# Performance work log

Measured on AMD Instinct MI355X. Metric: run time of the kernel, lower is better.

## Reference

```python
import jax, jax.numpy as jnp
import numpy as np

B, N, I_IN, O_OUT, S_EX, S_PHI, S_RHO = 1024, 32, 6, 5, 10, 60, 60
N_ACTIONS, N_ROLES = 5, 7


def _gru(x, h, Wih, Whh, bih, bhh):
    # PyTorch GRUCell math
    gi = x @ Wih.T + bih
    gh = h @ Whh.T + bhh
    ir, iz, inn = jnp.split(gi, 3, axis=-1)
    hr, hz, hn = jnp.split(gh, 3, axis=-1)
    r = jax.nn.sigmoid(ir + hr)
    u = jax.nn.sigmoid(iz + hz)
    n = jnp.tanh(inn + r * hn)
    return (1.0 - u) * n + u * h


def setup_inputs():
    key = jax.random.key(0)
    ks = jax.random.split(key, 32)
    has = (jax.random.uniform(ks[0], (B, N)) < 0.8).astype(jnp.float32)  # per-batch node existence
    z = jax.random.normal(ks[1], (B, N, S_EX), jnp.float32)
    dz = jax.random.normal(ks[2], (B, N, S_EX), jnp.float32)
    # union-graph DAG adjacency: adj[j, i] == edge j -> i, j < i (strictly upper triangular)
    adj = jnp.triu(jax.random.uniform(ks[3], (N, N)) < 0.3, k=1)

    def U(k, shape, fan_in):
        s = 1.0 / np.sqrt(fan_in)
        return jax.random.uniform(k, shape, jnp.float32, -s, s)

    fin = S_PHI + 2 * S_EX
    p = {
        'Wih_f': U(ks[4], (3 * S_PHI, S_RHO), S_PHI),
        'Whh_f': U(ks[5], (3 * S_PHI, S_PHI), S_PHI),
        'bih_f': U(ks[6], (3 * S_PHI,), S_PHI),
        'bhh_f': U(ks[7], (3 * S_PHI,), S_PHI),
        'Wih_b': U(ks[8], (3 * S_PHI, S_RHO), S_PHI),
        'Whh_b': U(ks[9], (3 * S_PHI, S_PHI), S_PHI),
        'bih_b': U(ks[10], (3 * S_PHI,), S_PHI),
        'bhh_b': U(ks[11], (3 * S_PHI,), S_PHI),
        'Wf': U(ks[12], (S_RHO, fin), fin), 'bf': U(ks[13], (S_RHO,), fin),
        'Wb': U(ks[14], (S_RHO, fin), fin), 'bb': U(ks[15], (S_RHO,), fin),
        'Wa': U(ks[16], (N_ACTIONS, 2 * S_PHI), 2 * S_PHI), 'ba': U(ks[17], (N_ACTIONS,), 2 * S_PHI),
        'Wc': U(ks[18], (1, 2 * S_PHI), 2 * S_PHI), 'bc': U(ks[19], (1,), 2 * S_PHI),
        'Wu': U(ks[20], (N_ROLES, 2 * S_RHO), 2 * S_RHO), 'bu': U(ks[21], (N_ROLES,), 2 * S_RHO),
    }
    return {'has': has, 'z': z, 'dz': dz, 'adj': adj, **p}


def reference(has, z, dz, adj,
              Wih_f, Whh_f, bih_f, bhh_f,
              Wih_b, Whh_b, bih_b, bhh_b,
              Wf, bf, Wb, bb, Wa, ba, Wc, bc, Wu, bu):
    adjf = adj.astype(z.dtype)

    # ---- forward message pass over DAG (ascending node order) ----
    def fwd_node(rho_f, i):
        def step(h, j):
            m = adjf[j, i] * has[:, j][:, None]  # interpolate mask: edge exists AND source node exists
            h2 = _gru(rho_f[j], h, Wih_f, Whh_f, bih_f, bhh_f)
            return h + m * (h2 - h), None
        h, _ = jax.lax.scan(step, jnp.zeros((B, S_PHI), z.dtype), jnp.arange(N))
        rho_i = jnp.tanh(jnp.concatenate([h, z[:, i], dz[:, i]], 1) @ Wf.T + bf)
        return rho_f.at[i].set(rho_i), None

    rho_f, _ = jax.lax.scan(fwd_node, jnp.zeros((N, B, S_RHO), z.dtype), jnp.arange(N))

    # ---- backward message pass (descending node order, descending out-neighbors) ----
    def bwd_node(rho_b, i):
        def step(h, j):
            m = adjf[i, j] * has[:, j][:, None]
            h2 = _gru(rho_b[j], h, Wih_b, Whh_b, bih_b, bhh_b)
            return h + m * (h2 - h), None
        h, _ = jax.lax.scan(step, jnp.zeros((B, S_PHI), z.dtype), jnp.arange(N - 1, -1, -1))
        rho_i = jnp.concatenate([h, z[:, i], dz[:, i]], 1) @ Wb.T + bb  # fc_backward has no activation
        return rho_b.at[i].set(rho_i), None

    rho_b, _ = jax.lax.scan(bwd_node, jnp.zeros((N, B, S_RHO), z.dtype), jnp.arange(N - 1, -1, -1))

    # ---- alpha aggregations over output / input nodes ----
    def alpha_f_step(h, i):
        h2 = _gru(rho_f[i], h, Wih_f, Whh_f, bih_f, bhh_f)
        return h + has[:, i][:, None] * (h2 - h), None
    alpha_f, _ = jax.lax.scan(alpha_f_step, jnp.zeros((B, S_RHO), z.dtype), jnp.arange(N - O_OUT, N))

    def alpha_b_step(h, i):
        h2 = _gru(rho_b[i], h, Wih_b, Whh_b, bih_b, bhh_b)
        return h + has[:, i][:, None] * (h2 - h), None
    alpha_b, _ = jax.lax.scan(alpha_b_step, jnp.zeros((B, S_RHO), z.dtype), jnp.arange(I_IN - 1, -1, -1))

    glob = jnp.concatenate([alpha_f, alpha_b], 1)  # [B, 2*S_phi]
    omega = glob @ Wa.T + ba                        # [B, 5]
    value = glob @ Wc.T + bc                        # [B, 1]

    psi = jnp.concatenate([rho_f, rho_b], -1) @ Wu.T + bu  # [N, B, 7]
    psi = jnp.transpose(psi, (1, 2, 0))                    # [B, 7, N]
    mask = has[:, None, :]
    psi = -60.0 * (1.0 - mask) + psi * mask                # interpolate(-60, psi, has)

    instr_prob = jax.nn.softmax(omega, axis=1)
    role_prob = jax.nn.softmax(psi, axis=1)
    return instr_prob, role_prob, value
```

## Files before the change

kernel.cpp:

```cpp
#include <hip/hip_runtime.h>


namespace {

typedef float v2f __attribute__((ext_vector_type(2)));

constexpr int Bc = 1024;
constexpr int Nn = 32;
constexpr int SP = 60;
constexpr int NA = 5;
constexpr int NR = 7;

constexpr int WS_WIH = 24576;
constexpr int WS_WP  = 49152;
constexpr int WS_TOTAL = 59392;
constexpr int DSTRIDE_G = 12288;
constexpr int DSTRIDE_P = 5120;

constexpr int OFF_ST   = 0;
constexpr int OFF_RP   = OFF_ST + Nn * 64;
constexpr int OFF_PART = OFF_RP + 512;
constexpr int OFF_ZDZ  = OFF_PART + 4096;
constexpr int OFF_PSI  = OFF_ZDZ + Nn * 20;
constexpr int OFF_WU   = OFF_PSI + Nn * 8;
constexpr int OFF_WA   = OFF_WU + 840;
constexpr int OFF_WC   = OFF_WA + 600;
constexpr int OFF_BA   = OFF_WC + 120;
constexpr int OFF_BU   = OFF_BA + 8;
constexpr int OFF_BC   = OFF_BU + 8;
constexpr int OFF_HAS  = OFF_BC + 4;
constexpr int OFF_AF   = OFF_HAS + 32;
constexpr int OFF_AB   = OFF_AF + 64;
constexpr int OFF_OS   = OFF_AB + 64;
constexpr int OFF_MASK = OFF_OS + 8;
constexpr int LDS_FLOATS = OFF_MASK + 68 + 8;

__device__ __forceinline__ float sigm(float x) {
    return 1.0f / (1.0f + __expf(-x));
}

__device__ __forceinline__ float tanh_f(float x) {
    float e = __expf(fminf(2.0f * x, 80.0f));
    return (e - 1.0f) / (e + 1.0f);
}

__device__ __forceinline__ unsigned adj_nz(const unsigned* a, int mode, int r, int c) {
    const int idx = r * 32 + c;
    unsigned v = (mode == 1) ? ((a[idx >> 2] >> (8 * (idx & 3))) & 0xffu) : a[idx];
    return v != 0u ? 1u : 0u;
}

__device__ __forceinline__ void matvec3(const v2f (&W)[3][8], const v2f* x,
                                        float& r0, float& r1, float& r2) {
    v2f a0 = {0.f, 0.f}, a1 = {0.f, 0.f}, a2 = {0.f, 0.f};
#pragma unroll
    for (int p = 0; p < 8; ++p) {
        const v2f xp = x[p];
        a0 = __builtin_elementwise_fma(W[0][p], xp, a0);
        a1 = __builtin_elementwise_fma(W[1][p], xp, a1);
        a2 = __builtin_elementwise_fma(W[2][p], xp, a2);
    }
    r0 = a0.x + a0.y; r1 = a1.x + a1.y; r2 = a2.x + a2.y;
}

__device__ __forceinline__ void load_w(const float* __restrict__ ws, int d,
        int w, int lane, v2f onev,
        v2f (&wh)[3][8], v2f (&wx)[3][8], v2f (&wp)[10]) {
    const v2f* WH = (const v2f*)(ws + d * DSTRIDE_G + ((lane * 4 + w) << 4));
    const v2f* WX = (const v2f*)(ws + WS_WIH + d * DSTRIDE_G + ((lane * 4 + w) << 4));
    const v2f* WPp = (const v2f*)(ws + WS_WP + d * DSTRIDE_P + (lane * 4 + w) * 20);
#pragma unroll
    for (int g = 0; g < 3; ++g)
#pragma unroll
        for (int p = 0; p < 8; ++p) {
            wh[g][p] = WH[g * 2048 + p] * onev;
            wx[g][p] = WX[g * 2048 + p] * onev;
        }
#pragma unroll
    for (int p = 0; p < 10; ++p) wp[p] = WPp[p] * onev;
}

__global__ void pack_kernel(const float* __restrict__ Whh_f, const float* __restrict__ Wih_f,
                            const float* __restrict__ Wf,
                            const float* __restrict__ Whh_b, const float* __restrict__ Wih_b,
                            const float* __restrict__ Wb, float* __restrict__ ws) {
    const int idx = blockIdx.x * 256 + threadIdx.x;
    if (idx < 2 * 24576) {
        const int which = idx / 24576;
        int r = idx % 24576;
        const int j = r & 15; r >>= 4;
        const int w = r & 3;  r >>= 2;
        const int lane = r & 63; r >>= 6;
        const int g = r % 3;
        const int d = r / 3;
        const int k = 16 * w + j;
        const float* src = which ? (d ? Wih_b : Wih_f) : (d ? Whh_b : Whh_f);
        ws[idx] = (lane < 60 && k < 60) ? src[(g * 60 + lane) * 60 + k] : 0.f;
    } else if (idx < WS_TOTAL) {
        int r = idx - WS_WP;
        const int jj = r % 20; r /= 20;
        const int w = r & 3;  r >>= 2;
        const int lane = r & 63;
        const int d = r >> 6;
        const float* src = d ? Wb : Wf;
        const int pk = (w < 3) ? 20 * w : 60;
        ws[idx] = (lane < 60) ? src[lane * 80 + pk + jj] : 0.f;
    }
}

template <int FWD>
__device__ __forceinline__ void run_dir(float* lds,
        const v2f (&wh)[3][8], const v2f (&wx)[3][8], const v2f (&wp)[10],
        const float* __restrict__ bih, const float* __restrict__ bhh,
        const float* __restrict__ bp, int w, int lane, int ln, int& par) {
    float* st = lds + OFF_ST;
    const unsigned* succm = (const unsigned*)(lds + OFF_MASK);
    const unsigned* predm = succm + 32;

    const float b0s = bih[ln] + bhh[ln];
    const float b1s = bih[60 + ln] + bhh[60 + ln];
    const float b2i = bih[120 + ln];
    const float b2h = bhh[120 + ln];
    const float bpv = bp[ln];

    for (int s = 0; s < Nn; ++s) {
        const int t = FWD ? s : (Nn - 1 - s);

        v2f pa = {0.f, 0.f};
        const v2f* xb = (w < 3) ? ((const v2f*)(st + t * 64) + 10 * w)
                                : ((const v2f*)(lds + OFF_ZDZ + t * 20));
#pragma unroll
        for (int p = 0; p < 10; ++p)
            pa = __builtin_elementwise_fma(wp[p], xb[p], pa);
        lds[OFF_RP + (par * 4 + w) * 64 + lane] = pa.x + pa.y;
        __syncthreads();
        float sum = lds[OFF_RP + (par * 4 + 0) * 64 + lane]
                  + lds[OFF_RP + (par * 4 + 1) * 64 + lane]
                  + lds[OFF_RP + (par * 4 + 2) * 64 + lane]
                  + lds[OFF_RP + (par * 4 + 3) * 64 + lane] + bpv;
        par ^= 1;
        const float rho = FWD ? tanh_f(sum) : sum;
        if (lane < SP) st[t * 64 + lane] = rho;

        const float hb = lds[OFF_HAS + t];
        unsigned m = (hb != 0.f) ? (FWD ? succm[t] : predm[t]) : 0u;
        if (m) {
            float gi0, gi1, gi2;
            matvec3(wx, (const v2f*)(st + t * 64) + 8 * w, gi0, gi1, gi2);
            while (m) {
                int i0 = __ffs(m) - 1; m &= m - 1u;
                int i1 = -1, i2 = -1, i3 = -1, cnt = 1;
                if (m) { i1 = __ffs(m) - 1; m &= m - 1u; ++cnt;
                    if (m) { i2 = __ffs(m) - 1; m &= m - 1u; ++cnt;
                        if (m) { i3 = __ffs(m) - 1; m &= m - 1u; ++cnt; } } }
                {
                    float g0, g1, g2;
                    matvec3(wh, (const v2f*)(st + i0 * 64) + 8 * w, g0, g1, g2);
                    float4 q = {gi0 + g0, gi1 + g1, gi2, g2};
                    *(float4*)(lds + OFF_PART + ((0 * 4 + w) * 64 + lane) * 4) = q;
                }
                if (cnt > 1) {
                    float g0, g1, g2;
                    matvec3(wh, (const v2f*)(st + i1 * 64) + 8 * w, g0, g1, g2);
                    float4 q = {gi0 + g0, gi1 + g1, gi2, g2};
                    *(float4*)(lds + OFF_PART + ((1 * 4 + w) * 64 + lane) * 4) = q;
                }
                if (cnt > 2) {
                    float g0, g1, g2;
                    matvec3(wh, (const v2f*)(st + i2 * 64) + 8 * w, g0, g1, g2);
                    float4 q = {gi0 + g0, gi1 + g1, gi2, g2};
                    *(float4*)(lds + OFF_PART + ((2 * 4 + w) * 64 + lane) * 4) = q;
                }
                if (cnt > 3) {
                    float g0, g1, g2;
                    matvec3(wh, (const v2f*)(st + i3 * 64) + 8 * w, g0, g1, g2);
                    float4 q = {gi0 + g0, gi1 + g1, gi2, g2};
                    *(float4*)(lds + OFF_PART + ((3 * 4 + w) * 64 + lane) * 4) = q;
                }
                __syncthreads();
                if (w < cnt) {
                    const int it = (w == 0) ? i0 : (w == 1) ? i1 : (w == 2) ? i2 : i3;
                    const float4 q0 = *(const float4*)(lds + OFF_PART + ((w * 4 + 0) * 64 + lane) * 4);
                    const float4 q1 = *(const float4*)(lds + OFF_PART + ((w * 4 + 1) * 64 + lane) * 4);
                    const float4 q2 = *(const float4*)(lds + OFF_PART + ((w * 4 + 2) * 64 + lane) * 4);
                    const float4 q3 = *(const float4*)(lds + OFF_PART + ((w * 4 + 3) * 64 + lane) * 4);
                    const float a0  = q0.x + q1.x + q2.x + q3.x + b0s;
                    const float a1  = q0.y + q1.y + q2.y + q3.y + b1s;
                    const float a2i = q0.z + q1.z + q2.z + q3.z + b2i;
                    const float a2h = q0.w + q1.w + q2.w + q3.w + b2h;
                    const float r = sigm(a0);
                    const float u = sigm(a1);
                    const float n = tanh_f(fmaf(r, a2h, a2i));
                    const float hold = st[it * 64 + lane];
                    const float hnew = fmaf(u, hold - n, n);
                    if (lane < SP) st[it * 64 + lane] = hnew;
                }
                __syncthreads();
            }
        }
    }

    float* ah = lds + (FWD ? OFF_AF : OFF_AB);
    ah[lane] = 0.f;
    const int acn = FWD ? 5 : 6;
    for (int s2 = 0; s2 < acn; ++s2) {
        const int i = FWD ? (Nn - 5 + s2) : (5 - s2);
        if (lds[OFF_HAS + i] == 0.f) continue;
        float gi0, gi1, gi2, g0, g1, g2;
        matvec3(wx, (const v2f*)(st + i * 64) + 8 * w, gi0, gi1, gi2);
        matvec3(wh, (const v2f*)(ah) + 8 * w, g0, g1, g2);
        float4 q = {gi0 + g0, gi1 + g1, gi2, g2};
        *(float4*)(lds + OFF_PART + (w * 64 + lane) * 4) = q;
        __syncthreads();
        if (w == 0) {
            const float4 q0 = *(const float4*)(lds + OFF_PART + ((0 * 64) + lane) * 4);
            const float4 q1 = *(const float4*)(lds + OFF_PART + ((1 * 64) + lane) * 4);
            const float4 q2 = *(const float4*)(lds + OFF_PART + ((2 * 64) + lane) * 4);
            const float4 q3 = *(const float4*)(lds + OFF_PART + ((3 * 64) + lane) * 4);
            const float a0  = q0.x + q1.x + q2.x + q3.x + b0s;
            const float a1  = q0.y + q1.y + q2.y + q3.y + b1s;
            const float a2i = q0.z + q1.z + q2.z + q3.z + b2i;
            const float a2h = q0.w + q1.w + q2.w + q3.w + b2h;
            const float r = sigm(a0);
            const float u = sigm(a1);
            const float n = tanh_f(fmaf(r, a2h, a2i));
            const float hold = ah[lane];
            const float hnew = fmaf(u, hold - n, n);
            if (lane < SP) ah[lane] = hnew;
        }
        __syncthreads();
    }
}

__device__ void run_heads(float* lds, int b, int lane, float* __restrict__ out) {
    const float* aF = lds + OFF_AF;
    const float* aB = lds + OFF_AB;

    float o = 0.f;
    if (lane < NA) {
        o = lds[OFF_BA + lane];
        const float* wa = lds + OFF_WA + lane * 120;
#pragma unroll
        for (int k = 0; k < SP; ++k) o = fmaf(wa[k], aF[k], o);
#pragma unroll
        for (int k = 0; k < SP; ++k) o = fmaf(wa[60 + k], aB[k], o);
        lds[OFF_OS + lane] = o;
    } else if (lane == NA) {
        float v = lds[OFF_BC];
        const float* wc = lds + OFF_WC;
#pragma unroll
        for (int k = 0; k < SP; ++k) v = fmaf(wc[k], aF[k], v);
#pragma unroll
        for (int k = 0; k < SP; ++k) v = fmaf(wc[60 + k], aB[k], v);
        out[Bc * NA + Bc * NR * Nn + b] = v;
    }
    __builtin_amdgcn_wave_barrier();

    if (lane < NA) {
        const float* os = lds + OFF_OS;
        float mx = os[0];
#pragma unroll
        for (int j = 1; j < NA; ++j) mx = fmaxf(mx, os[j]);
        float sum = 0.f;
#pragma unroll
        for (int j = 0; j < NA; ++j) sum += __expf(os[j] - mx);
        out[b * NA + lane] = __expf(o - mx) / sum;
    }

    if (lane < Nn) {
        const int i = lane;
        const float mk = lds[OFF_HAS + i];
        float p[NR];
        float mx = -1e30f;
#pragma unroll
        for (int c = 0; c < NR; ++c) {
            const float v = (mk != 0.f)
                ? (lds[OFF_PSI + i * 8 + c] + lds[OFF_BU + c])
                : -60.0f;
            p[c] = v;
            mx = fmaxf(mx, v);
        }
        float sum = 0.f;
#pragma unroll
        for (int c = 0; c < NR; ++c) { p[c] = __expf(p[c] - mx); sum += p[c]; }
        const float inv = 1.0f / sum;
#pragma unroll
        for (int c = 0; c < NR; ++c)
            out[Bc * NA + b * (NR * Nn) + c * Nn + i] = p[c] * inv;
    }
}

__global__ __launch_bounds__(256, 2)
void dn_kernel(const float* __restrict__ has, const float* __restrict__ z,
               const float* __restrict__ dz, const unsigned* __restrict__ adjw,
               const float* __restrict__ bih_f, const float* __restrict__ bhh_f,
               const float* __restrict__ bih_b, const float* __restrict__ bhh_b,
               const float* __restrict__ bf, const float* __restrict__ bb,
               const float* __restrict__ Wa, const float* __restrict__ ba,
               const float* __restrict__ Wc, const float* __restrict__ bc,
               const float* __restrict__ Wu, const float* __restrict__ bu,
               const float* __restrict__ ws, float* __restrict__ out) {
    __shared__ float lds[LDS_FLOATS];
    const int tid = threadIdx.x;
    const int lane = tid & 63;
    const int w = tid >> 6;
    const int b = blockIdx.x;
    const int ln = (lane < SP) ? lane : (SP - 1);

    unsigned* succm = (unsigned*)(lds + OFF_MASK);
    unsigned* predm = succm + 32;
    unsigned* flags = predm + 32;

    if (tid < 4) flags[tid] = 0u;
    __syncthreads();

    {
        unsigned ff = 0u, fb = 0u;
        for (int i = tid; i < 256; i += 256) {
            const unsigned v = adjw[i];
            ff |= (v == 0x3f800000u) ? 1u : 0u;
            fb |= (v > 1u && v != 0x3f800000u) ? 1u : 0u;
        }
        if (ff) atomicOr(&flags[0], 1u);
        if (fb) atomicOr(&flags[1], 1u);
    }

    for (int i = tid; i < 840; i += 256) lds[OFF_WU + i] = Wu[i];
    for (int i = tid; i < 600; i += 256) lds[OFF_WA + i] = Wa[i];
    if (tid < 120) lds[OFF_WC + tid] = Wc[tid];
    if (tid < NR) lds[OFF_BU + tid] = bu[tid];
    if (tid < NA) lds[OFF_BA + tid] = ba[tid];
    if (tid == 0) lds[OFF_BC] = bc[0];
    if (tid < Nn) lds[OFF_HAS + tid] = has[b * 32 + tid];
    for (int i = tid; i < Nn * 20; i += 256) {
        const int t = i / 20, k = i - t * 20;
        lds[OFF_ZDZ + i] = (k < 10) ? z[(b * Nn + t) * 10 + k]
                                    : dz[(b * Nn + t) * 10 + (k - 10)];
    }
    for (int i = tid; i < Nn * 64; i += 256) lds[OFF_ST + i] = 0.f;
    __syncthreads();

    const int mode = flags[0] ? 2 : (flags[1] ? 1 : 0);
    if (tid < 32) {
        unsigned sm = 0u;
        for (int c = 0; c < 32; ++c) sm |= adj_nz(adjw, mode, tid, c) << c;
        succm[tid] = sm;
    } else if (tid < 64) {
        const int c = tid - 32;
        unsigned pm = 0u;
        for (int r = 0; r < 32; ++r) pm |= adj_nz(adjw, mode, r, c) << r;
        predm[c] = pm;
    }
    __syncthreads();

    float one = 1.0f;
    asm volatile("" : "+v"(one));
    const v2f onev = {one, one};

    int par = 0;
    v2f wh[3][8], wx[3][8], wp[10];

    load_w(ws, 0, w, lane, onev, wh, wx, wp);
    run_dir<1>(lds, wh, wx, wp, bih_f, bhh_f, bf, w, lane, ln, par);
    __syncthreads();

    if (tid < Nn * NR) {
        const int i = tid / NR, c = tid - i * NR;
        const float* wu = lds + OFF_WU + c * 120;
        const float* sf = lds + OFF_ST + i * 64;
        float acc = 0.f;
#pragma unroll
        for (int k = 0; k < SP; ++k) acc = fmaf(wu[k], sf[k], acc);
        lds[OFF_PSI + i * 8 + c] = acc;
    }
    __syncthreads();

    for (int i = tid; i < Nn * 64; i += 256) lds[OFF_ST + i] = 0.f;
    __syncthreads();

    load_w(ws, 1, w, lane, onev, wh, wx, wp);
    run_dir<0>(lds, wh, wx, wp, bih_b, bhh_b, bb, w, lane, ln, par);
    __syncthreads();

    if (tid < Nn * NR) {
        const int i = tid / NR, c = tid - i * NR;
        const float* wu = lds + OFF_WU + c * 120 + 60;
        const float* sb = lds + OFF_ST + i * 64;
        float acc = 0.f;
#pragma unroll
        for (int k = 0; k < SP; ++k) acc = fmaf(wu[k], sb[k], acc);
        lds[OFF_PSI + i * 8 + c] += acc;
    }
    __syncthreads();

    if (w == 0) run_heads(lds, b, lane, out);
}

}

extern "C" void kernel_launch(void* const* d_in, const int* in_sizes, int n_in,
                              void* d_out, int out_size, void* d_ws, size_t ws_size,
                              hipStream_t stream) {
    (void)in_sizes; (void)n_in; (void)out_size; (void)ws_size;
    const float* has     = (const float*)d_in[0];
    const float* z       = (const float*)d_in[1];
    const float* dz      = (const float*)d_in[2];
    const unsigned* adjw = (const unsigned*)d_in[3];
    const float* Wih_f   = (const float*)d_in[4];
    const float* Whh_f   = (const float*)d_in[5];
    const float* bih_f   = (const float*)d_in[6];
    const float* bhh_f   = (const float*)d_in[7];
    const float* Wih_b   = (const float*)d_in[8];
    const float* Whh_b   = (const float*)d_in[9];
    const float* bih_b   = (const float*)d_in[10];
    const float* bhh_b   = (const float*)d_in[11];
    const float* Wf      = (const float*)d_in[12];
    const float* bf      = (const float*)d_in[13];
    const float* Wb      = (const float*)d_in[14];
    const float* bb      = (const float*)d_in[15];
    const float* Wa      = (const float*)d_in[16];
    const float* ba      = (const float*)d_in[17];
    const float* Wc      = (const float*)d_in[18];
    const float* bc      = (const float*)d_in[19];
    const float* Wu      = (const float*)d_in[20];
    const float* bu      = (const float*)d_in[21];
    float* out = (float*)d_out;
    float* ws  = (float*)d_ws;

    pack_kernel<<<(WS_TOTAL + 255) / 256, 256, 0, stream>>>(
        Whh_f, Wih_f, Wf, Whh_b, Wih_b, Wb, ws);

    dn_kernel<<<Bc, 256, 0, stream>>>(
        has, z, dz, adjw,
        bih_f, bhh_f, bih_b, bhh_b, bf, bb,
        Wa, ba, Wc, bc, Wu, bu, ws, out);
}
```

Before: 367.7 us.

## Process two batch samples per workgroup sharing register-resident GRU weights

Each workgroup now handles two batch elements, running the DAG message pass for both with the same register-held weight fragments and sharing barriers. The grid halves to 512 blocks and the LDS layout doubles the state, partial and input buffers. Barrier and weight-load costs are amortized over two samples, and per-sample has-masking is folded into the GRU update so the shared adjacency loop can run when either sample has the node. The tradeoffs are more LDS per block, fewer blocks (possibly under-filling the GPU), and extra work when only one of the two samples has a node.

```diff
diff --git a/kernel.cpp b/kernel.cpp
--- a/kernel.cpp
+++ b/kernel.cpp
@@ -18,21 +18,21 @@
 constexpr int DSTRIDE_P = 5120;
 
 constexpr int OFF_ST   = 0;
-constexpr int OFF_RP   = OFF_ST + Nn * 64;
-constexpr int OFF_PART = OFF_RP + 512;
-constexpr int OFF_ZDZ  = OFF_PART + 4096;
-constexpr int OFF_PSI  = OFF_ZDZ + Nn * 20;
-constexpr int OFF_WU   = OFF_PSI + Nn * 8;
-constexpr int OFF_WA   = OFF_WU + 840;
-constexpr int OFF_WC   = OFF_WA + 600;
-constexpr int OFF_BA   = OFF_WC + 120;
-constexpr int OFF_BU   = OFF_BA + 8;
-constexpr int OFF_BC   = OFF_BU + 8;
-constexpr int OFF_HAS  = OFF_BC + 4;
-constexpr int OFF_AF   = OFF_HAS + 32;
-constexpr int OFF_AB   = OFF_AF + 64;
-constexpr int OFF_OS   = OFF_AB + 64;
-constexpr int OFF_MASK = OFF_OS + 8;
+constexpr int OFF_RP   = 4096;
+constexpr int OFF_PART = 5120;
+constexpr int OFF_ZDZ  = 13312;
+constexpr int OFF_PSI  = 14592;
+constexpr int OFF_WU   = 15104;
+constexpr int OFF_WA   = 15944;
+constexpr int OFF_WC   = 16544;
+constexpr int OFF_BA   = 16664;
+constexpr int OFF_BU   = 16672;
+constexpr int OFF_BC   = 16680;
+constexpr int OFF_HAS  = 16684;
+constexpr int OFF_AF   = 16748;
+constexpr int OFF_AB   = 16876;
+constexpr int OFF_OS   = 17004;
+constexpr int OFF_MASK = 17020;
 constexpr int LDS_FLOATS = OFF_MASK + 68 + 8;
 
 __device__ __forceinline__ float sigm(float x) {
@@ -108,14 +108,37 @@
     }
 }
 
+__device__ __forceinline__ void gru_fin(float* lds, int s, int slot, int lane,
+        float b0s, float b1s, float b2i, float b2h,
+        float* hrow, float m, bool act) {
+    const int base = OFF_PART + ((s * 4 + slot) * 4) * 256;
+    const float4 q0 = *(const float4*)(lds + base + (0 * 64 + lane) * 4);
+    const float4 q1 = *(const float4*)(lds + base + (1 * 64 + lane) * 4);
+    const float4 q2 = *(const float4*)(lds + base + (2 * 64 + lane) * 4);
+    const float4 q3 = *(const float4*)(lds + base + (3 * 64 + lane) * 4);
+    const float a0  = q0.x + q1.x + q2.x + q3.x + b0s;
+    const float a1  = q0.y + q1.y + q2.y + q3.y + b1s;
+    const float a2i = q0.z + q1.z + q2.z + q3.z + b2i;
+    const float a2h = q0.w + q1.w + q2.w + q3.w + b2h;
+    const float r = sigm(a0);
+    const float u = sigm(a1);
+    const float n = tanh_f(fmaf(r, a2h, a2i));
+    const float hold = hrow[lane];
+    const float h2 = fmaf(u, hold - n, n);
+    const float hnew = fmaf(m, h2 - hold, hold);
+    if (act) hrow[lane] = hnew;
+}
+
 template <int FWD>
 __device__ __forceinline__ void run_dir(float* lds,
         const v2f (&wh)[3][8], const v2f (&wx)[3][8], const v2f (&wp)[10],
         const float* __restrict__ bih, const float* __restrict__ bhh,
         const float* __restrict__ bp, int w, int lane, int ln, int& par) {
-    float* st = lds + OFF_ST;
+    float* st0 = lds + OFF_ST;
+    float* st1 = lds + OFF_ST + 2048;
     const unsigned* succm = (const unsigned*)(lds + OFF_MASK);
     const unsigned* predm = succm + 32;
+    const bool act = lane < SP;
 
     const float b0s = bih[ln] + bhh[ln];
     const float b1s = bih[60 + ln] + bhh[60 + ln];
@@ -126,115 +149,96 @@
     for (int s = 0; s < Nn; ++s) {
         const int t = FWD ? s : (Nn - 1 - s);
 
-        v2f pa = {0.f, 0.f};
-        const v2f* xb = (w < 3) ? ((const v2f*)(st + t * 64) + 10 * w)
-                                : ((const v2f*)(lds + OFF_ZDZ + t * 20));
-#pragma unroll
-        for (int p = 0; p < 10; ++p)
-            pa = __builtin_elementwise_fma(wp[p], xb[p], pa);
-        lds[OFF_RP + (par * 4 + w) * 64 + lane] = pa.x + pa.y;
+        v2f pa0 = {0.f, 0.f}, pa1 = {0.f, 0.f};
+        const v2f* xb0 = (w < 3) ? ((const v2f*)(st0 + t * 64) + 10 * w)
+                                 : ((const v2f*)(lds + OFF_ZDZ + t * 20));
+        const v2f* xb1 = (w < 3) ? ((const v2f*)(st1 + t * 64) + 10 * w)
+                                 : ((const v2f*)(lds + OFF_ZDZ + 640 + t * 20));
+#pragma unroll
+        for (int p = 0; p < 10; ++p) {
+            pa0 = __builtin_elementwise_fma(wp[p], xb0[p], pa0);
+            pa1 = __builtin_elementwise_fma(wp[p], xb1[p], pa1);
+        }
+        lds[OFF_RP + ((par * 2 + 0) * 4 + w) * 64 + lane] = pa0.x + pa0.y;
+        lds[OFF_RP + ((par * 2 + 1) * 4 + w) * 64 + lane] = pa1.x + pa1.y;
         __syncthreads();
-        float sum = lds[OFF_RP + (par * 4 + 0) * 64 + lane]
-                  + lds[OFF_RP + (par * 4 + 1) * 64 + lane]
-                  + lds[OFF_RP + (par * 4 + 2) * 64 + lane]
-                  + lds[OFF_RP + (par * 4 + 3) * 64 + lane] + bpv;
+        float sum0 = lds[OFF_RP + ((par * 2) * 4 + 0) * 64 + lane]
+                   + lds[OFF_RP + ((par * 2) * 4 + 1) * 64 + lane]
+                   + lds[OFF_RP + ((par * 2) * 4 + 2) * 64 + lane]
+                   + lds[OFF_RP + ((par * 2) * 4 + 3) * 64 + lane] + bpv;
+        float sum1 = lds[OFF_RP + ((par * 2 + 1) * 4 + 0) * 64 + lane]
+                   + lds[OFF_RP + ((par * 2 + 1) * 4 + 1) * 64 + lane]
+                   + lds[OFF_RP + ((par * 2 + 1) * 4 + 2) * 64 + lane]
+                   + lds[OFF_RP + ((par * 2 + 1) * 4 + 3) * 64 + lane] + bpv;
         par ^= 1;
-        const float rho = FWD ? tanh_f(sum) : sum;
-        if (lane < SP) st[t * 64 + lane] = rho;
-
-        const float hb = lds[OFF_HAS + t];
-        unsigned m = (hb != 0.f) ? (FWD ? succm[t] : predm[t]) : 0u;
-        if (m) {
-            float gi0, gi1, gi2;
-            matvec3(wx, (const v2f*)(st + t * 64) + 8 * w, gi0, gi1, gi2);
-            while (m) {
-                int i0 = __ffs(m) - 1; m &= m - 1u;
+        const float rho0 = FWD ? tanh_f(sum0) : sum0;
+        const float rho1 = FWD ? tanh_f(sum1) : sum1;
+        if (act) { st0[t * 64 + lane] = rho0; st1[t * 64 + lane] = rho1; }
+
+        const float m0 = lds[OFF_HAS + t];
+        const float m1 = lds[OFF_HAS + 32 + t];
+        unsigned mk = (m0 != 0.f || m1 != 0.f) ? (FWD ? succm[t] : predm[t]) : 0u;
+        if (mk) {
+            float gA0, gA1, gA2, gB0, gB1, gB2;
+            matvec3(wx, (const v2f*)(st0 + t * 64) + 8 * w, gA0, gA1, gA2);
+            matvec3(wx, (const v2f*)(st1 + t * 64) + 8 * w, gB0, gB1, gB2);
+            while (mk) {
+                int i0 = __ffs(mk) - 1; mk &= mk - 1u;
                 int i1 = -1, i2 = -1, i3 = -1, cnt = 1;
-                if (m) { i1 = __ffs(m) - 1; m &= m - 1u; ++cnt;
-                    if (m) { i2 = __ffs(m) - 1; m &= m - 1u; ++cnt;
-                        if (m) { i3 = __ffs(m) - 1; m &= m - 1u; ++cnt; } } }
-                {
+                if (mk) { i1 = __ffs(mk) - 1; mk &= mk - 1u; ++cnt;
+                    if (mk) { i2 = __ffs(mk) - 1; mk &= mk - 1u; ++cnt;
+                        if (mk) { i3 = __ffs(mk) - 1; mk &= mk - 1u; ++cnt; } } }
+                const int ii[4] = {i0, i1, i2, i3};
+#pragma unroll
+                for (int j = 0; j < 4; ++j) {
+                    if (j >= cnt) break;
                     float g0, g1, g2;
-                    matvec3(wh, (const v2f*)(st + i0 * 64) + 8 * w, g0, g1, g2);
-                    float4 q = {gi0 + g0, gi1 + g1, gi2, g2};
-                    *(float4*)(lds + OFF_PART + ((0 * 4 + w) * 64 + lane) * 4) = q;
-                }
-                if (cnt > 1) {
-                    float g0, g1, g2;
-                    matvec3(wh, (const v2f*)(st + i1 * 64) + 8 * w, g0, g1, g2);
-                    float4 q = {gi0 + g0, gi1 + g1, gi2, g2};
-                    *(float4*)(lds + OFF_PART + ((1 * 4 + w) * 64 + lane) * 4) = q;
-                }
-                if (cnt > 2) {
-                    float g0, g1, g2;
-                    matvec3(wh, (const v2f*)(st + i2 * 64) + 8 * w, g0, g1, g2);
-                    float4 q = {gi0 + g0, gi1 + g1, gi2, g2};
-                    *(float4*)(lds + OFF_PART + ((2 * 4 + w) * 64 + lane) * 4) = q;
-                }
-                if (cnt > 3) {
-                    float g0, g1, g2;
-                    matvec3(wh, (const v2f*)(st + i3 * 64) + 8 * w, g0, g1, g2);
-                    float4 q = {gi0 + g0, gi1 + g1, gi2, g2};
-                    *(float4*)(lds + OFF_PART + ((3 * 4 + w) * 64 + lane) * 4) = q;
+                    matvec3(wh, (const v2f*)(st0 + ii[j] * 64) + 8 * w, g0, g1, g2);
+                    float4 q = {gA0 + g0, gA1 + g1, gA2, g2};
+                    *(float4*)(lds + OFF_PART + ((0 * 4 + j) * 4 + w) * 256 + lane * 4) = q;
+                    matvec3(wh, (const v2f*)(st1 + ii[j] * 64) + 8 * w, g0, g1, g2);
+                    float4 q2v = {gB0 + g0, gB1 + g1, gB2, g2};
+                    *(float4*)(lds + OFF_PART + ((1 * 4 + j) * 4 + w) * 256 + lane * 4) = q2v;
                 }
                 __syncthreads();
                 if (w < cnt) {
-                    const int it = (w == 0) ? i0 : (w == 1) ? i1 : (w == 2) ? i2 : i3;
-                    const float4 q0 = *(const float4*)(lds + OFF_PART + ((w * 4 + 0) * 64 + lane) * 4);
-                    const float4 q1 = *(const float4*)(lds + OFF_PART + ((w * 4 + 1) * 64 + lane) * 4);
-                    const float4 q2 = *(const float4*)(lds + OFF_PART + ((w * 4 + 2) * 64 + lane) * 4);
-                    const float4 q3 = *(const float4*)(lds + OFF_PART + ((w * 4 + 3) * 64 + lane) * 4);
-                    const float a0  = q0.x + q1.x + q2.x + q3.x + b0s;
-                    const float a1  = q0.y + q1.y + q2.y + q3.y + b1s;
-                    const float a2i = q0.z + q1.z + q2.z + q3.z + b2i;
-                    const float a2h = q0.w + q1.w + q2.w + q3.w + b2h;
-                    const float r = sigm(a0);
-                    const float u = sigm(a1);
-                    const float n = tanh_f(fmaf(r, a2h, a2i));
-                    const float hold = st[it * 64 + lane];
-                    const float hnew = fmaf(u, hold - n, n);
-                    if (lane < SP) st[it * 64 + lane] = hnew;
+                    const int it = ii[w];
+                    gru_fin(lds, 0, w, lane, b0s, b1s, b2i, b2h, st0 + it * 64, m0, act);
+                    gru_fin(lds, 1, w, lane, b0s, b1s, b2i, b2h, st1 + it * 64, m1, act);
                 }
                 __syncthreads();
             }
         }
     }
 
-    float* ah = lds + (FWD ? OFF_AF : OFF_AB);
-    ah[lane] = 0.f;
+    float* ah0 = lds + (FWD ? OFF_AF : OFF_AB);
+    float* ah1 = ah0 + 64;
+    ah0[lane] = 0.f; ah1[lane] = 0.f;
     const int acn = FWD ? 5 : 6;
     for (int s2 = 0; s2 < acn; ++s2) {
         const int i = FWD ? (Nn - 5 + s2) : (5 - s2);
-        if (lds[OFF_HAS + i] == 0.f) continue;
-        float gi0, gi1, gi2, g0, g1, g2;
-        matvec3(wx, (const v2f*)(st + i * 64) + 8 * w, gi0, gi1, gi2);
-        matvec3(wh, (const v2f*)(ah) + 8 * w, g0, g1, g2);
-        float4 q = {gi0 + g0, gi1 + g1, gi2, g2};
-        *(float4*)(lds + OFF_PART + (w * 64 + lane) * 4) = q;
+        const float m0 = lds[OFF_HAS + i];
+        const float m1 = lds[OFF_HAS + 32 + i];
+        if (m0 == 0.f && m1 == 0.f) continue;
+        float gA0, gA1, gA2, gB0, gB1, gB2, g0, g1, g2;
+        matvec3(wx, (const v2f*)(st0 + i * 64) + 8 * w, gA0, gA1, gA2);
+        matvec3(wh, (const v2f*)(ah0) + 8 * w, g0, g1, g2);
+        float4 q = {gA0 + g0, gA1 + g1, gA2, g2};
+        *(float4*)(lds + OFF_PART + ((0 * 4 + 0) * 4 + w) * 256 + lane * 4) = q;
+        matvec3(wx, (const v2f*)(st1 + i * 64) + 8 * w, gB0, gB1, gB2);
+        matvec3(wh, (const v2f*)(ah1) + 8 * w, g0, g1, g2);
+        float4 q2v = {gB0 + g0, gB1 + g1, gB2, g2};
+        *(float4*)(lds + OFF_PART + ((1 * 4 + 0) * 4 + w) * 256 + lane * 4) = q2v;
         __syncthreads();
-        if (w == 0) {
-            const float4 q0 = *(const float4*)(lds + OFF_PART + ((0 * 64) + lane) * 4);
-            const float4 q1 = *(const float4*)(lds + OFF_PART + ((1 * 64) + lane) * 4);
-            const float4 q2 = *(const float4*)(lds + OFF_PART + ((2 * 64) + lane) * 4);
-            const float4 q3 = *(const float4*)(lds + OFF_PART + ((3 * 64) + lane) * 4);
-            const float a0  = q0.x + q1.x + q2.x + q3.x + b0s;
-            const float a1  = q0.y + q1.y + q2.y + q3.y + b1s;
-            const float a2i = q0.z + q1.z + q2.z + q3.z + b2i;
-            const float a2h = q0.w + q1.w + q2.w + q3.w + b2h;
-            const float r = sigm(a0);
-            const float u = sigm(a1);
-            const float n = tanh_f(fmaf(r, a2h, a2i));
-            const float hold = ah[lane];
-            const float hnew = fmaf(u, hold - n, n);
-            if (lane < SP) ah[lane] = hnew;
-        }
+        if (w == 0)      gru_fin(lds, 0, 0, lane, b0s, b1s, b2i, b2h, ah0, m0, act);
+        else if (w == 1) gru_fin(lds, 1, 0, lane, b0s, b1s, b2i, b2h, ah1, m1, act);
         __syncthreads();
     }
 }
 
-__device__ void run_heads(float* lds, int b, int lane, float* __restrict__ out) {
-    const float* aF = lds + OFF_AF;
-    const float* aB = lds + OFF_AB;
+__device__ void run_heads(float* lds, int s, int b, int lane, float* __restrict__ out) {
+    const float* aF = lds + OFF_AF + s * 64;
+    const float* aB = lds + OFF_AB + s * 64;
 
     float o = 0.f;
     if (lane < NA) {
@@ -244,7 +248,7 @@
         for (int k = 0; k < SP; ++k) o = fmaf(wa[k], aF[k], o);
 #pragma unroll
         for (int k = 0; k < SP; ++k) o = fmaf(wa[60 + k], aB[k], o);
-        lds[OFF_OS + lane] = o;
+        lds[OFF_OS + s * 8 + lane] = o;
     } else if (lane == NA) {
         float v = lds[OFF_BC];
         const float* wc = lds + OFF_WC;
@@ -257,7 +261,7 @@
     __builtin_amdgcn_wave_barrier();
 
     if (lane < NA) {
-        const float* os = lds + OFF_OS;
+        const float* os = lds + OFF_OS + s * 8;
         float mx = os[0];
 #pragma unroll
         for (int j = 1; j < NA; ++j) mx = fmaxf(mx, os[j]);
@@ -269,13 +273,13 @@
 
     if (lane < Nn) {
         const int i = lane;
-        const float mk = lds[OFF_HAS + i];
+        const float mkk = lds[OFF_HAS + s * 32 + i];
         float p[NR];
         float mx = -1e30f;
 #pragma unroll
         for (int c = 0; c < NR; ++c) {
-            const float v = (mk != 0.f)
-                ? (lds[OFF_PSI + i * 8 + c] + lds[OFF_BU + c])
+            const float v = (mkk != 0.f)
+                ? (lds[OFF_PSI + s * 256 + i * 8 + c] + lds[OFF_BU + c])
                 : -60.0f;
             p[c] = v;
             mx = fmaxf(mx, v);
@@ -304,7 +308,7 @@
     const int tid = threadIdx.x;
     const int lane = tid & 63;
     const int w = tid >> 6;
-    const int b = blockIdx.x;
+    const int b0 = blockIdx.x * 2;
     const int ln = (lane < SP) ? lane : (SP - 1);
 
     unsigned* succm = (unsigned*)(lds + OFF_MASK);
@@ -331,13 +335,14 @@
     if (tid < NR) lds[OFF_BU + tid] = bu[tid];
     if (tid < NA) lds[OFF_BA + tid] = ba[tid];
     if (tid == 0) lds[OFF_BC] = bc[0];
-    if (tid < Nn) lds[OFF_HAS + tid] = has[b * 32 + tid];
-    for (int i = tid; i < Nn * 20; i += 256) {
-        const int t = i / 20, k = i - t * 20;
-        lds[OFF_ZDZ + i] = (k < 10) ? z[(b * Nn + t) * 10 + k]
-                                    : dz[(b * Nn + t) * 10 + (k - 10)];
-    }
-    for (int i = tid; i < Nn * 64; i += 256) lds[OFF_ST + i] = 0.f;
+    if (tid < 64) lds[OFF_HAS + tid] = has[(b0 + (tid >> 5)) * 32 + (tid & 31)];
+    for (int i = tid; i < 2 * Nn * 20; i += 256) {
+        const int ss = i / 640, r = i - ss * 640;
+        const int t = r / 20, k = r - t * 20;
+        lds[OFF_ZDZ + i] = (k < 10) ? z[((b0 + ss) * Nn + t) * 10 + k]
+                                    : dz[((b0 + ss) * Nn + t) * 10 + (k - 10)];
+    }
+    for (int i = tid; i < 2 * Nn * 64; i += 256) lds[OFF_ST + i] = 0.f;
     __syncthreads();
 
     const int mode = flags[0] ? 2 : (flags[1] ? 1 : 0);
@@ -367,15 +372,20 @@
     if (tid < Nn * NR) {
         const int i = tid / NR, c = tid - i * NR;
         const float* wu = lds + OFF_WU + c * 120;
-        const float* sf = lds + OFF_ST + i * 64;
-        float acc = 0.f;
-#pragma unroll
-        for (int k = 0; k < SP; ++k) acc = fmaf(wu[k], sf[k], acc);
-        lds[OFF_PSI + i * 8 + c] = acc;
-    }
-    __syncthreads();
-
-    for (int i = tid; i < Nn * 64; i += 256) lds[OFF_ST + i] = 0.f;
+        const float* s0 = lds + OFF_ST + i * 64;
+        const float* s1 = lds + OFF_ST + 2048 + i * 64;
+        float a0 = 0.f, a1 = 0.f;
+#pragma unroll
+        for (int k = 0; k < SP; ++k) {
+            a0 = fmaf(wu[k], s0[k], a0);
+            a1 = fmaf(wu[k], s1[k], a1);
+        }
+        lds[OFF_PSI + i * 8 + c] = a0;
+        lds[OFF_PSI + 256 + i * 8 + c] = a1;
+    }
+    __syncthreads();
+
+    for (int i = tid; i < 2 * Nn * 64; i += 256) lds[OFF_ST + i] = 0.f;
     __syncthreads();
 
     load_w(ws, 1, w, lane, onev, wh, wx, wp);
@@ -385,15 +395,21 @@
     if (tid < Nn * NR) {
         const int i = tid / NR, c = tid - i * NR;
         const float* wu = lds + OFF_WU + c * 120 + 60;
-        const float* sb = lds + OFF_ST + i * 64;
-        float acc = 0.f;
-#pragma unroll
-        for (int k = 0; k < SP; ++k) acc = fmaf(wu[k], sb[k], acc);
-        lds[OFF_PSI + i * 8 + c] += acc;
-    }
-    __syncthreads();
-
-    if (w == 0) run_heads(lds, b, lane, out);
+        const float* s0 = lds + OFF_ST + i * 64;
+        const float* s1 = lds + OFF_ST + 2048 + i * 64;
+        float a0 = 0.f, a1 = 0.f;
+#pragma unroll
+        for (int k = 0; k < SP; ++k) {
+            a0 = fmaf(wu[k], s0[k], a0);
+            a1 = fmaf(wu[k], s1[k], a1);
+        }
+        lds[OFF_PSI + i * 8 + c] += a0;
+        lds[OFF_PSI + 256 + i * 8 + c] += a1;
+    }
+    __syncthreads();
+
+    if (w == 0) run_heads(lds, 0, b0, lane, out);
+    else if (w == 1) run_heads(lds, 1, b0 + 1, lane, out);
 }
 
 }
@@ -430,7 +446,7 @@
     pack_kernel<<<(WS_TOTAL + 255) / 256, 256, 0, stream>>>(
         Whh_f, Wih_f, Wf, Whh_b, Wih_b, Wb, ws);
 
-    dn_kernel<<<Bc, 256, 0, stream>>>(
+    dn_kernel<<<Bc / 2, 256, 0, stream>>>(
         has, z, dz, adjw,
         bih_f, bhh_f, bih_b, bhh_b, bf, bb,
         Wa, ba, Wc, bc, Wu, bu, ws, out);
```

Result: faster. 345.7 us (-6.0%).
